# Optimization experiments

Hardware: AMD Instinct MI355X
Metric: run time of the kernel (lower is better)

The kernel has to match this reference:

```python
import jax, jax.numpy as jnp
import numpy as np

NEG_SLOPE = 0.01
EPS = 1e-8


def _conv2d(x, w, b, pad):
    y = jax.lax.conv_general_dilated(
        x, w, window_strides=(1, 1), padding=[(pad, pad), (pad, pad)],
        dimension_numbers=("NCHW", "OIHW", "NCHW"))
    return y + b[None, :, None, None]


def _leaky(x):
    return jnp.where(x >= 0, x, NEG_SLOPE * x)


def _maxpool2(x):
    return jax.lax.reduce_window(x, -jnp.inf, jax.lax.max,
                                 (1, 1, 2, 2), (1, 1, 2, 2), "VALID")


def _upsample2(x):  # nearest, scale_factor=2 (matches F.interpolate default)
    return jnp.repeat(jnp.repeat(x, 2, axis=2), 2, axis=3)


def _forward(x1, x2, pts1, enc, dec):
    B, L = pts1.shape[:2]
    H, W = x1.shape[-2:]
    h1, h2 = x1, x2
    pts = pts1.astype(jnp.int32)
    attns, feats = [], []
    for (w, b) in enc:
        Hi, Wi = h1.shape[-2:]
        h1 = _leaky(_conv2d(h1, w, b, 2))
        h2 = _leaky(_conv2d(h2, w, b, 2))
        feats.append(h2)
        h1 = _maxpool2(h1)
        h2 = _maxpool2(h2)
        C_, Hi_, Wi_ = h1.shape[-3:]
        # pts[...,0] = pts[...,0]*Hi_//Hi ; same for W (integer floor)
        pts = jnp.stack([(pts[..., 0] * Hi_) // Hi, (pts[..., 1] * Wi_) // Wi], axis=-1)
        idx = pts[..., 0] * Wi_ + pts[..., 1]  # (B, L)
        h1f = h1.reshape(B, C_, Hi_ * Wi_)
        h2f = h2.reshape(B, C_, Hi_ * Wi_)
        query = jnp.take_along_axis(h1f, jnp.broadcast_to(idx[:, None, :], (B, C_, L)), axis=2)  # (B, C, L)
        # cosine similarity between every pixel of h2 and every query point
        dots = jnp.einsum("bcp,bcl->bpl", h2f, query)
        n2 = jnp.maximum(jnp.linalg.norm(h2f, axis=1), EPS)    # (B, P)
        nq = jnp.maximum(jnp.linalg.norm(query, axis=1), EPS)  # (B, L)
        attn = dots / (n2[:, :, None] * nq[:, None, :])        # (B, P, L)
        attn = attn.reshape(B, Hi_, Wi_, L).transpose(0, 3, 1, 2).reshape(B * L, 1, Hi_, Wi_)
        attns.append(attn)
    h2 = jnp.tile(h2, (L, 1, 1, 1))  # torch .repeat(L,1,1,1)
    n_dec = len(dec)
    for i, (w, b) in enumerate(dec):
        j = len(enc) - i - 1
        h2 = jnp.concatenate([h2, attns[j]], axis=1)
        h2 = _upsample2(h2)
        feat = jnp.tile(feats[j], (L, 1, 1, 1))
        h2 = jnp.concatenate([h2, feat], axis=1)
        h2 = _conv2d(h2, w, b, 1)
        if i < n_dec - 1:
            h2 = _leaky(h2)
    return h2.reshape(B, L, H, W)


def setup_inputs() -> dict:
    key = jax.random.key(0)
    ks = jax.random.split(key, 24)
    B, L, H, W = 2, 32, 256, 256
    inp = {
        "x1": jax.random.uniform(ks[0], (B, 3, H, W), dtype=jnp.float32),
        "x2": jax.random.uniform(ks[1], (B, 3, H, W), dtype=jnp.float32),
        "pts1": jax.random.randint(ks[2], (B, L, 2), 0, H, dtype=jnp.int32),
    }
    enc_shapes = [(4, 3), (8, 4), (16, 8), (16, 16)]
    dec_shapes = [(16, 33), (8, 33), (4, 17), (1, 9)]
    k = 3
    for i, (co, ci) in enumerate(enc_shapes):
        inp[f"enc_w{i}"] = jax.random.normal(ks[k], (co, ci, 5, 5), dtype=jnp.float32) * 0.05
        inp[f"enc_b{i}"] = jnp.zeros((co,), dtype=jnp.float32)
        k += 1
    for i, (co, ci) in enumerate(dec_shapes):
        inp[f"dec_w{i}"] = jax.random.normal(ks[k], (co, ci, 3, 3), dtype=jnp.float32) * 0.05
        inp[f"dec_b{i}"] = jnp.zeros((co,), dtype=jnp.float32)
        k += 1
    return inp


def reference(x1, x2, pts1,
              enc_w0, enc_b0, enc_w1, enc_b1, enc_w2, enc_b2, enc_w3, enc_b3,
              dec_w0, dec_b0, dec_w1, dec_b1, dec_w2, dec_b2, dec_w3, dec_b3):
    enc = [(enc_w0, enc_b0), (enc_w1, enc_b1), (enc_w2, enc_b2), (enc_w3, enc_b3)]
    dec = [(dec_w0, dec_b0), (dec_w1, dec_b1), (dec_w2, dec_b2), (dec_w3, dec_b3)]
    return _forward(x1, x2, pts1, enc, dec)
```

## Files before the change

kernel.cpp:

```cpp
#include <hip/hip_runtime.h>
#include <cstdint>

__device__ __forceinline__ float leaky(float v) { return v >= 0.f ? v : 0.01f * v; }

__global__ void __launch_bounds__(256) enc0_k(
    const float* __restrict__ x1, const float* __restrict__ x2,
    const float* __restrict__ w, const float* __restrict__ bias,
    float* __restrict__ c2, float* __restrict__ pout)
{
    constexpr int R = 256;
    __shared__ float ss[3 * 36 * 36];
    __shared__ float ws[4 * 3 * 25 + 4];
    int t = threadIdx.x;
    int n = blockIdx.y;
    int tileY = blockIdx.x >> 3, tileX = blockIdx.x & 7;
    int Y0 = 32 * tileY, X0 = 32 * tileX;
    const float* src = (n < 2) ? x1 + (size_t)n * 3 * R * R
                               : x2 + (size_t)(n - 2) * 3 * R * R;

    for (int i = t; i < 300; i += 256) ws[i] = w[i];
    if (t < 4) ws[300 + t] = bias[t];
    for (int ci = 0; ci < 3; ++ci) {
        const float* sp = src + (size_t)ci * R * R;
        for (int i = t; i < 1296; i += 256) {
            int r = i / 36, col = i - r * 36;
            int gy = Y0 - 2 + r, gx = X0 - 2 + col;
            float v = 0.f;
            if (gy >= 0 && gy < R && gx >= 0 && gx < R) v = sp[gy * R + gx];
            ss[ci * 1296 + i] = v;
        }
    }
    __syncthreads();

    int qx = t & 15, qy = t >> 4;
    float acc[4][2][2];
#pragma unroll
    for (int co = 0; co < 4; ++co) {
        float b0 = ws[300 + co];
        acc[co][0][0] = b0; acc[co][0][1] = b0; acc[co][1][0] = b0; acc[co][1][1] = b0;
    }
#pragma unroll
    for (int ci = 0; ci < 3; ++ci) {
        const float* sp = &ss[ci * 1296 + (2 * qy) * 36 + 2 * qx];
        float S[6][6];
#pragma unroll
        for (int i = 0; i < 6; ++i)
#pragma unroll
            for (int j = 0; j < 6; ++j) S[i][j] = sp[i * 36 + j];
#pragma unroll
        for (int co = 0; co < 4; ++co) {
#pragma unroll
            for (int dy = 0; dy < 5; ++dy) {
#pragma unroll
                for (int dx = 0; dx < 5; ++dx) {
                    float wv = ws[(co * 3 + ci) * 25 + dy * 5 + dx];
                    acc[co][0][0] = fmaf(wv, S[dy][dx],         acc[co][0][0]);
                    acc[co][0][1] = fmaf(wv, S[dy][dx + 1],     acc[co][0][1]);
                    acc[co][1][0] = fmaf(wv, S[dy + 1][dx],     acc[co][1][0]);
                    acc[co][1][1] = fmaf(wv, S[dy + 1][dx + 1], acc[co][1][1]);
                }
            }
        }
    }
#pragma unroll
    for (int co = 0; co < 4; ++co) {
        float v00 = leaky(acc[co][0][0]), v01 = leaky(acc[co][0][1]);
        float v10 = leaky(acc[co][1][0]), v11 = leaky(acc[co][1][1]);
        if (n >= 2) {
            float* op = c2 + ((size_t)((n - 2) * 4 + co)) * R * R + (Y0 + 2 * qy) * R + X0 + 2 * qx;
            float2 a; a.x = v00; a.y = v01; *(float2*)op = a;
            float2 b2; b2.x = v10; b2.y = v11; *(float2*)(op + R) = b2;
        }
        float pv = fmaxf(fmaxf(v00, v01), fmaxf(v10, v11));
        pout[((size_t)(n * 4 + co)) * 16384 + (16 * tileY + qy) * 128 + 16 * tileX + qx] = pv;
    }
}

template<int R, int CI, int CO, int COG>
__device__ __forceinline__ void enc_body(
    const float* __restrict__ src1, const float* __restrict__ src2,
    const float* __restrict__ w, const float* __restrict__ bias,
    float* __restrict__ c2, float* __restrict__ pout, int bx)
{
    constexpr int W = R, H = R, Wt = R / 2;
    constexpr int RPB = 256 / Wt;
    __shared__ float ws[COG * CI * 25];
    __shared__ float pl[(RPB / 2) * COG * Wt];

    int t = threadIdx.x;
    int gid = bx * 256 + t;
    int col = gid % Wt;
    int y = (gid / Wt) % H;
    int n = (gid / (Wt * H)) & 3;
    int g = gid / (Wt * H * 4);

    if (COG == 2) {
        for (int i = t; i < COG * CI * 25; i += 256) {
            int cg = i & 1, idx = i >> 1;
            ws[idx * 2 + cg] = w[(g * COG + cg) * CI * 25 + idx];
        }
    } else {
        for (int i = t; i < COG * CI * 25; i += 256) ws[i] = w[g * COG * CI * 25 + i];
    }
    __syncthreads();

    const float* sp = (n < 2) ? (src1 + (size_t)n * CI * H * W)
                              : (src2 + (size_t)(n - 2) * CI * H * W);
    int x0 = col * 2;

    float acc[COG][2];
#pragma unroll
    for (int cg = 0; cg < COG; ++cg) { float b0 = bias[g * COG + cg]; acc[cg][0] = b0; acc[cg][1] = b0; }

    bool okr[5], okc[3];
#pragma unroll
    for (int i = 0; i < 5; ++i) { int yy = y + i - 2; okr[i] = (yy >= 0) && (yy < H); }
#pragma unroll
    for (int j = 0; j < 3; ++j) { int xx = x0 + 2 * j - 2; okc[j] = (xx >= 0) && (xx < W); }

#pragma unroll 4
    for (int ci = 0; ci < CI; ++ci) {
        const float* s = sp + ci * H * W + (y - 2) * W + (x0 - 2);
        float p[5][6];
#pragma unroll
        for (int i = 0; i < 5; ++i) {
#pragma unroll
            for (int j = 0; j < 3; ++j) {
                if (okr[i] & okc[j]) {
                    float2 v = *(const float2*)(s + i * W + 2 * j);
                    p[i][2 * j] = v.x; p[i][2 * j + 1] = v.y;
                } else { p[i][2 * j] = 0.f; p[i][2 * j + 1] = 0.f; }
            }
        }
        if (COG == 2) {
#pragma unroll
            for (int dy = 0; dy < 5; ++dy) {
#pragma unroll
                for (int dx = 0; dx < 5; ++dx) {
                    float2 wv = *(const float2*)&ws[(ci * 25 + dy * 5 + dx) * 2];
                    acc[0][0] = fmaf(wv.x, p[dy][dx],     acc[0][0]);
                    acc[0][1] = fmaf(wv.x, p[dy][dx + 1], acc[0][1]);
                    acc[1][0] = fmaf(wv.y, p[dy][dx],     acc[1][0]);
                    acc[1][1] = fmaf(wv.y, p[dy][dx + 1], acc[1][1]);
                }
            }
        } else {
#pragma unroll
            for (int cg = 0; cg < COG; ++cg) {
#pragma unroll
                for (int dy = 0; dy < 5; ++dy) {
#pragma unroll
                    for (int dx = 0; dx < 5; ++dx) {
                        float wv = ws[(cg * CI + ci) * 25 + dy * 5 + dx];
                        acc[cg][0] = fmaf(wv, p[dy][dx],     acc[cg][0]);
                        acc[cg][1] = fmaf(wv, p[dy][dx + 1], acc[cg][1]);
                    }
                }
            }
        }
    }

    int r = t / Wt;
    float m[COG];
#pragma unroll
    for (int cg = 0; cg < COG; ++cg) {
        float v0 = leaky(acc[cg][0]), v1 = leaky(acc[cg][1]);
        m[cg] = fmaxf(v0, v1);
        if (n >= 2) {
            float2 stv; stv.x = v0; stv.y = v1;
            *(float2*)(c2 + ((size_t)((n - 2) * CO + g * COG + cg)) * H * W + y * W + x0) = stv;
        }
    }
    if (r & 1) {
#pragma unroll
        for (int cg = 0; cg < COG; ++cg)
            pl[((r >> 1) * COG + cg) * Wt + col] = m[cg];
    }
    __syncthreads();
    if (!(r & 1)) {
#pragma unroll
        for (int cg = 0; cg < COG; ++cg) {
            float pv = fmaxf(m[cg], pl[((r >> 1) * COG + cg) * Wt + col]);
            pout[((size_t)(n * CO + g * COG + cg)) * Wt * Wt + (y >> 1) * Wt + col] = pv;
        }
    }
}

template<int R, int CI, int CO, int COG>
__global__ void __launch_bounds__(256) enc_k(
    const float* __restrict__ src1, const float* __restrict__ src2,
    const float* __restrict__ w, const float* __restrict__ bias,
    float* __restrict__ c2, float* __restrict__ pout)
{
    enc_body<R, CI, CO, COG>(src1, src2, w, bias, c2, pout, blockIdx.x);
}

template<int C, int RP, int SHIFT>
__device__ __forceinline__ void attn_body(
    const float* __restrict__ pool, const int* __restrict__ pts,
    float* __restrict__ out, int tile, int b)
{
    constexpr int P = RP * RP;
    __shared__ float qs[32 * C];
    int t = threadIdx.x;
    if (t < 32) {
        int l = t;
        int py = pts[(b * 32 + l) * 2 + 0] >> SHIFT;
        int px = pts[(b * 32 + l) * 2 + 1] >> SHIFT;
        const float* qp = pool + (size_t)(b * C) * P + py * RP + px;
        float v[C]; float s = 0.f;
#pragma unroll
        for (int c = 0; c < C; ++c) { v[c] = qp[c * P]; s += v[c] * v[c]; }
        float invn = 1.f / fmaxf(sqrtf(s), 1e-8f);
#pragma unroll
        for (int c = 0; c < C; ++c) qs[l * C + c] = v[c] * invn;
    }
    __syncthreads();
    int p = tile * 256 + t;
    const float* hp = pool + (size_t)((2 + b) * C) * P + p;
    float v[C]; float s = 0.f;
#pragma unroll
    for (int c = 0; c < C; ++c) { v[c] = hp[c * P]; s += v[c] * v[c]; }
    float invn2 = 1.f / fmaxf(sqrtf(s), 1e-8f);
#pragma unroll 4
    for (int l = 0; l < 32; ++l) {
        float d = 0.f;
#pragma unroll
        for (int c = 0; c < C; ++c) d = fmaf(v[c], qs[l * C + c], d);
        out[(size_t)(b * 32 + l) * P + p] = d * invn2;
    }
}

template<int R, int CI, int CINW, int CO, int COG>
__device__ __forceinline__ void fb_body(
    const float* __restrict__ in, const float* __restrict__ w,
    const float* __restrict__ bias, float* __restrict__ fb,
    int par, int tile, int cog)
{
    constexpr int QD = R / 2;
    __shared__ float ws[COG * CI * 9];
    int t = threadIdx.x;
    for (int i = t; i < COG * CI * 9; i += 256) {
        int co = i / (CI * 9), rem = i - co * (CI * 9);
        ws[i] = w[(cog * COG + co) * CINW * 9 + (CINW - CI) * 9 + rem];
    }
    __syncthreads();
    int q = tile * 256 + t;
    int qx = q % QD, qy = q / QD;
    const float* ip = in + (size_t)par * CI * R * R;
    float acc[COG][2][2];
#pragma unroll
    for (int co = 0; co < COG; ++co) {
        float b0 = bias[cog * COG + co];
        acc[co][0][0] = b0; acc[co][0][1] = b0; acc[co][1][0] = b0; acc[co][1][1] = b0;
    }
    bool fr[4], fc[4];
#pragma unroll
    for (int i = 0; i < 4; ++i) {
        int yy = 2 * qy - 1 + i; fr[i] = (yy >= 0) && (yy < R);
        int xx = 2 * qx - 1 + i; fc[i] = (xx >= 0) && (xx < R);
    }
#pragma unroll 4
    for (int ci = 0; ci < CI; ++ci) {
        const float* bp = ip + (size_t)ci * R * R + (2 * qy - 1) * R + (2 * qx - 1);
        float F[4][4];
#pragma unroll
        for (int i = 0; i < 4; ++i)
#pragma unroll
            for (int j = 0; j < 4; ++j)
                F[i][j] = (fr[i] & fc[j]) ? bp[i * R + j] : 0.f;
#pragma unroll
        for (int co = 0; co < COG; ++co) {
#pragma unroll
            for (int dy = 0; dy < 3; ++dy) {
#pragma unroll
                for (int dx = 0; dx < 3; ++dx) {
                    float wv = ws[(co * CI + ci) * 9 + dy * 3 + dx];
                    acc[co][0][0] = fmaf(wv, F[dy][dx],         acc[co][0][0]);
                    acc[co][0][1] = fmaf(wv, F[dy][dx + 1],     acc[co][0][1]);
                    acc[co][1][0] = fmaf(wv, F[dy + 1][dx],     acc[co][1][0]);
                    acc[co][1][1] = fmaf(wv, F[dy + 1][dx + 1], acc[co][1][1]);
                }
            }
        }
    }
#pragma unroll
    for (int co = 0; co < COG; ++co) {
        float* op = fb + ((size_t)(par * CO + cog * COG + co)) * R * R + (2 * qy) * R + 2 * qx;
        float2 a; a.x = acc[co][0][0]; a.y = acc[co][0][1]; *(float2*)op = a;
        float2 b2; b2.x = acc[co][1][0]; b2.y = acc[co][1][1]; *(float2*)(op + R) = b2;
    }
}

__device__ __forceinline__ void fb0_body(
    const float* __restrict__ p3, const float* __restrict__ c2_3,
    const float* __restrict__ w, const float* __restrict__ bias,
    float* __restrict__ fb0, int par, int tile, int cog)
{
    __shared__ float ws0[4 * 33 * 9];
    int t = threadIdx.x;
    for (int i = t; i < 4 * 33 * 9; i += 256) ws0[i] = w[cog * 4 * 33 * 9 + i];
    __syncthreads();
    int px = tile * 256 + t;
    int x = px & 31, y = px >> 5;
    const float* prevp = p3 + (size_t)(2 + par) * 16 * 256;
    const float* featp = c2_3 + (size_t)par * 16 * 1024;
    float acc[4];
#pragma unroll
    for (int co = 0; co < 4; ++co) acc[co] = bias[cog * 4 + co];

    bool oky[3], okx[3];
    int py[3], pxh[3];
#pragma unroll
    for (int i = 0; i < 3; ++i) {
        int iy = y - 1 + i; oky[i] = (iy >= 0) && (iy < 32); py[i] = (iy >= 0 ? iy : 0) >> 1;
        int ix = x - 1 + i; okx[i] = (ix >= 0) && (ix < 32); pxh[i] = (ix >= 0 ? ix : 0) >> 1;
    }
#pragma unroll 4
    for (int ci = 0; ci < 16; ++ci) {
        const float* pp = prevp + ci * 256;
        float V[3][3];
#pragma unroll
        for (int i = 0; i < 3; ++i)
#pragma unroll
            for (int j = 0; j < 3; ++j)
                V[i][j] = (oky[i] & okx[j]) ? pp[py[i] * 16 + pxh[j]] : 0.f;
#pragma unroll
        for (int co = 0; co < 4; ++co) {
#pragma unroll
            for (int tap = 0; tap < 9; ++tap)
                acc[co] = fmaf(ws0[(co * 33 + ci) * 9 + tap], V[tap / 3][tap % 3], acc[co]);
        }
    }
#pragma unroll 4
    for (int cf = 0; cf < 16; ++cf) {
        const float* fp = featp + cf * 1024;
        float F[3][3];
#pragma unroll
        for (int i = 0; i < 3; ++i)
#pragma unroll
            for (int j = 0; j < 3; ++j) {
                int iy = y - 1 + i, ix = x - 1 + j;
                F[i][j] = (oky[i] & okx[j]) ? fp[iy * 32 + ix] : 0.f;
            }
#pragma unroll
        for (int co = 0; co < 4; ++co) {
#pragma unroll
            for (int tap = 0; tap < 9; ++tap)
                acc[co] = fmaf(ws0[(co * 33 + 17 + cf) * 9 + tap], F[tap / 3][tap % 3], acc[co]);
        }
    }
#pragma unroll
    for (int co = 0; co < 4; ++co)
        fb0[((size_t)(par * 16 + cog * 4 + co)) * 1024 + y * 32 + x] = acc[co];
}

__global__ void __launch_bounds__(256) bigprep_k(
    const float* __restrict__ p0, const float* __restrict__ p1,
    const float* __restrict__ p2, const int* __restrict__ pts,
    const float* __restrict__ ew3, const float* __restrict__ eb3,
    float* __restrict__ c2_3, float* __restrict__ p3,
    const float* __restrict__ c2_0, const float* __restrict__ c2_1,
    const float* __restrict__ c2_2,
    const float* __restrict__ dw1, const float* __restrict__ db1,
    const float* __restrict__ dw2, const float* __restrict__ db2,
    const float* __restrict__ dw3, const float* __restrict__ db3,
    float* __restrict__ at0, float* __restrict__ at1, float* __restrict__ at2,
    float* __restrict__ fb1, float* __restrict__ fb2, float* __restrict__ fb3)
{
    int bx = blockIdx.x;
    if (bx < 128) {
        enc_body<32, 16, 16, 1>(p2, p2 + (size_t)2 * 16 * 32 * 32, ew3, eb3, c2_3, p3, bx);
    } else if (bx < 256) {
        int r = bx - 128; attn_body<4, 128, 1>(p0, pts, at0, r >> 1, r & 1);
    } else if (bx < 288) {
        int r = bx - 256; attn_body<8, 64, 2>(p1, pts, at1, r >> 1, r & 1);
    } else if (bx < 296) {
        int r = bx - 288; attn_body<16, 32, 3>(p2, pts, at2, r >> 1, r & 1);
    } else if (bx < 424) {
        int sub = bx - 296; int par = sub >> 6, tile = sub & 63;
        fb_body<256, 4, 9, 1, 1>(c2_0, dw3, db3, fb3, par, tile, 0);
    } else if (bx < 456) {
        int sub = bx - 424; int par = sub >> 4, tile = sub & 15;
        fb_body<128, 8, 17, 4, 4>(c2_1, dw2, db2, fb2, par, tile, 0);
    } else {
        int sub = bx - 456; int cog = sub & 1, tile = (sub >> 1) & 3, par = sub >> 3;
        fb_body<64, 16, 33, 8, 4>(c2_2, dw1, db1, fb1, par, tile, cog);
    }
}

__global__ void __launch_bounds__(256) prep2_k(
    const float* __restrict__ p3, const float* __restrict__ c2_3,
    const int* __restrict__ pts,
    const float* __restrict__ dw0, const float* __restrict__ db0,
    float* __restrict__ at3, float* __restrict__ fb0)
{
    int bx = blockIdx.x;
    if (bx < 2) {
        attn_body<16, 16, 4>(p3, pts, at3, bx >> 1, bx & 1);
    } else {
        int sub = bx - 2; int cog = sub & 3, tile = (sub >> 2) & 3, par = sub >> 4;
        fb0_body(p3, c2_3, dw0, db0, fb0, par, tile, cog);
    }
}

__global__ void __launch_bounds__(256) dec0k_k(
    const float* __restrict__ at3, const float* __restrict__ fb0,
    const float* __restrict__ w, float* __restrict__ out)
{
    __shared__ float ws4[9 * 16];
    int t = threadIdx.x;
    if (t < 144) {
        int tap = t / 16, co = t - (t / 16) * 16;
        ws4[tap * 16 + co] = w[co * 33 * 9 + 16 * 9 + tap];
    }
    __syncthreads();
    int gid = blockIdx.x;
    int k = gid >> 2, tile = gid & 3;
    int px = tile * 256 + t;
    int x = px & 31, y = px >> 5;
    int par = k & 1;
    const float* ap = at3 + (size_t)k * 256;

    float A[3][3];
#pragma unroll
    for (int i = 0; i < 3; ++i) {
        int iy = y - 1 + i; bool oy = (iy >= 0) && (iy < 32); int py = (iy >= 0 ? iy : 0) >> 1;
#pragma unroll
        for (int j = 0; j < 3; ++j) {
            int ix = x - 1 + j; bool ox = (ix >= 0) && (ix < 32); int qx = (ix >= 0 ? ix : 0) >> 1;
            A[i][j] = (oy && ox) ? ap[py * 16 + qx] : 0.f;
        }
    }
    float acc[16];
#pragma unroll
    for (int co = 0; co < 16; ++co)
        acc[co] = fb0[((size_t)(par * 16 + co)) * 1024 + y * 32 + x];
#pragma unroll
    for (int tap = 0; tap < 9; ++tap) {
        float av = A[tap / 3][tap % 3];
#pragma unroll
        for (int c4 = 0; c4 < 4; ++c4) {
            float4 wv = *(const float4*)&ws4[tap * 16 + c4 * 4];
            acc[c4 * 4 + 0] = fmaf(wv.x, av, acc[c4 * 4 + 0]);
            acc[c4 * 4 + 1] = fmaf(wv.y, av, acc[c4 * 4 + 1]);
            acc[c4 * 4 + 2] = fmaf(wv.z, av, acc[c4 * 4 + 2]);
            acc[c4 * 4 + 3] = fmaf(wv.w, av, acc[c4 * 4 + 3]);
        }
    }
#pragma unroll
    for (int co = 0; co < 16; ++co)
        out[((size_t)(k * 16 + co)) * 1024 + y * 32 + x] = leaky(acc[co]);
}

__global__ void __launch_bounds__(256, 4) dec1k_k(
    const float* __restrict__ prev, const float* __restrict__ attn,
    const float* __restrict__ fb1, const float* __restrict__ w,
    float* __restrict__ out)
{
    constexpr int R = 64, CP = 16, CIN = 33, Rh = 32, CO = 8, COG = 4;
    __shared__ float ws[17 * 9 * COG];
    __shared__ float sh4[17 * 60 * 4];

    int t = threadIdx.x;
    int bz = blockIdx.y;
    int kg = bz >> 1, cog = bz & 1;
    int p = kg & 1;
    int kbase = (kg >> 1) * 8 + p;
    int tileY = blockIdx.x >> 2, tileX = blockIdx.x & 3;
    int Y0 = 8 * tileY, X0 = 16 * tileX;
    int hy0 = 4 * tileY - 1, hx0 = 8 * tileX - 1;

    for (int i = t; i < 17 * 9 * COG; i += 256) {
        int col = i & 3, idx = i >> 2;
        ws[idx * 4 + col] = w[(cog * COG + col) * CIN * 9 + idx];
    }
#pragma unroll 2
    for (int i = t; i < 17 * 60; i += 256) {
        int c = i / 60, rem = i - c * 60;
        int r = rem / 10, col = rem - r * 10;
        int gy = hy0 + r, gx = hx0 + col;
        bool ok = (gy >= 0) && (gy < Rh) && (gx >= 0) && (gx < Rh);
        int off = gy * Rh + gx;
        float4 v4; v4.x = 0.f; v4.y = 0.f; v4.z = 0.f; v4.w = 0.f;
        if (ok) {
            if (c < CP) {
                v4.x = prev[((size_t)((kbase + 0) * CP + c)) * Rh * Rh + off];
                v4.y = prev[((size_t)((kbase + 2) * CP + c)) * Rh * Rh + off];
                v4.z = prev[((size_t)((kbase + 4) * CP + c)) * Rh * Rh + off];
                v4.w = prev[((size_t)((kbase + 6) * CP + c)) * Rh * Rh + off];
            } else {
                v4.x = attn[(size_t)(kbase + 0) * Rh * Rh + off];
                v4.y = attn[(size_t)(kbase + 2) * Rh * Rh + off];
                v4.z = attn[(size_t)(kbase + 4) * Rh * Rh + off];
                v4.w = attn[(size_t)(kbase + 6) * Rh * Rh + off];
            }
        }
        *(float4*)&sh4[i * 4] = v4;
    }
    __syncthreads();

    int px = t & 127, copair = t >> 7;
    int qx = px & 15, qy = px >> 4;

    float acc[4][2];
#pragma unroll
    for (int c2 = 0; c2 < 2; ++c2) {
        float fv = fb1[((size_t)(p * CO + cog * COG + copair * 2 + c2)) * 4096 + (Y0 + qy) * R + X0 + qx];
#pragma unroll
        for (int j = 0; j < 4; ++j) acc[j][c2] = fv;
    }

    int rr[3] = {(qy + 1) >> 1, (qy + 2) >> 1, (qy + 3) >> 1};
    int cc[3] = {(qx + 1) >> 1, (qx + 2) >> 1, (qx + 3) >> 1};
    int pofs[3][3];
#pragma unroll
    for (int i = 0; i < 3; ++i)
#pragma unroll
        for (int j2 = 0; j2 < 3; ++j2)
            pofs[i][j2] = (rr[i] * 10 + cc[j2]) * 4;

#pragma unroll 4
    for (int ci = 0; ci < 17; ++ci) {
        const float* hp = &sh4[ci * 240];
        float4 P4[3][3];
#pragma unroll
        for (int i = 0; i < 3; ++i)
#pragma unroll
            for (int j2 = 0; j2 < 3; ++j2)
                P4[i][j2] = *(const float4*)&hp[pofs[i][j2]];
#pragma unroll
        for (int dy = 0; dy < 3; ++dy) {
#pragma unroll
            for (int dx = 0; dx < 3; ++dx) {
                float2 wv = *(const float2*)&ws[(ci * 9 + dy * 3 + dx) * 4 + copair * 2];
                acc[0][0] = fmaf(wv.x, P4[dy][dx].x, acc[0][0]);
                acc[1][0] = fmaf(wv.x, P4[dy][dx].y, acc[1][0]);
                acc[2][0] = fmaf(wv.x, P4[dy][dx].z, acc[2][0]);
                acc[3][0] = fmaf(wv.x, P4[dy][dx].w, acc[3][0]);
                acc[0][1] = fmaf(wv.y, P4[dy][dx].x, acc[0][1]);
                acc[1][1] = fmaf(wv.y, P4[dy][dx].y, acc[1][1]);
                acc[2][1] = fmaf(wv.y, P4[dy][dx].z, acc[2][1]);
                acc[3][1] = fmaf(wv.y, P4[dy][dx].w, acc[3][1]);
            }
        }
    }

#pragma unroll
    for (int j = 0; j < 4; ++j) {
        int k = kbase + 2 * j;
#pragma unroll
        for (int c2 = 0; c2 < 2; ++c2) {
            int co = cog * COG + copair * 2 + c2;
            out[((size_t)(k * CO + co)) * 4096 + (Y0 + qy) * R + X0 + qx] = leaky(acc[j][c2]);
        }
    }
}

template<int R, int CP, int CO, int CINW, int MINW, bool DOLEAKY>
__global__ void __launch_bounds__(256, MINW) dechalf_k(
    const float* __restrict__ prev, const float* __restrict__ attn,
    const float* __restrict__ fb, const float* __restrict__ w,
    float* __restrict__ out)
{
    constexpr int Rh = R / 2, TX = R / 16;
    constexpr bool PACKW = (CO == 4);
    __shared__ float sh[4][(CP + 1) * 100];
    __shared__ float ws4[PACKW ? (CP + 1) * 9 * 4 : 4];

    int t = threadIdx.x;
    int kg = blockIdx.y;
    int p = kg & 1;
    int kbase = (kg >> 1) * 8 + p;
    int tileY = blockIdx.x / TX, tileX = blockIdx.x % TX;
    int Y0 = 16 * tileY, X0 = 16 * tileX;
    int hy0 = 8 * tileY - 1, hx0 = 8 * tileX - 1;

    if (PACKW) {
        for (int i = t; i < (CP + 1) * 9 * 4; i += 256) {
            int co = i & 3, idx = i >> 2;
            ws4[i] = w[co * CINW * 9 + idx];
        }
    }
#pragma unroll 2
    for (int i = t; i < CP * 100; i += 256) {
        int c = i / 100, rem = i - c * 100;
        int r = rem / 10, col = rem - r * 10;
        int gy = hy0 + r, gx = hx0 + col;
        bool ok = (gy >= 0) && (gy < Rh) && (gx >= 0) && (gx < Rh);
        int off = gy * Rh + gx;
#pragma unroll
        for (int j = 0; j < 4; ++j) {
            float v = 0.f;
            if (ok) v = prev[((size_t)((kbase + 2 * j) * CP + c)) * Rh * Rh + off];
            sh[j][i] = v;
        }
    }
    if (t < 100) {
        int r = t / 10, col = t - r * 10;
        int gy = hy0 + r, gx = hx0 + col;
        bool ok = (gy >= 0) && (gy < Rh) && (gx >= 0) && (gx < Rh);
        int off = gy * Rh + gx;
#pragma unroll
        for (int j = 0; j < 4; ++j) {
            float v = 0.f;
            if (ok) v = attn[(size_t)(kbase + 2 * j) * Rh * Rh + off];
            sh[j][CP * 100 + t] = v;
        }
    }
    __syncthreads();

    int ksub = t >> 6, q = t & 63, qx = q & 7, qy = q >> 3;
    int k = kbase + 2 * ksub;

    float acc[CO][2][2];
#pragma unroll
    for (int co = 0; co < CO; ++co) {
        const float* fp = fb + ((size_t)(p * CO + co)) * R * R + (Y0 + 2 * qy) * R + X0 + 2 * qx;
        float2 r0 = *(const float2*)fp;
        float2 r1 = *(const float2*)(fp + R);
        acc[co][0][0] = r0.x; acc[co][0][1] = r0.y;
        acc[co][1][0] = r1.x; acc[co][1][1] = r1.y;
    }

#pragma unroll
    for (int ci = 0; ci < CP + 1; ++ci) {
        const float* hp = &sh[ksub][ci * 100 + qy * 10 + qx];
        float P[3][3];
#pragma unroll
        for (int i = 0; i < 3; ++i)
#pragma unroll
            for (int j = 0; j < 3; ++j) P[i][j] = hp[i * 10 + j];
#pragma unroll
        for (int dy = 0; dy < 3; ++dy) {
#pragma unroll
            for (int dx = 0; dx < 3; ++dx) {
                float p00 = P[(dy + 1) >> 1][(dx + 1) >> 1];
                float p01 = P[(dy + 1) >> 1][(dx + 2) >> 1];
                float p10 = P[(dy + 2) >> 1][(dx + 1) >> 1];
                float p11 = P[(dy + 2) >> 1][(dx + 2) >> 1];
                if (PACKW) {
                    float4 wv = *(const float4*)&ws4[(ci * 9 + dy * 3 + dx) * 4];
                    const float* wvp = (const float*)&wv;
#pragma unroll
                    for (int co = 0; co < CO; ++co) {
                        acc[co][0][0] = fmaf(wvp[co], p00, acc[co][0][0]);
                        acc[co][0][1] = fmaf(wvp[co], p01, acc[co][0][1]);
                        acc[co][1][0] = fmaf(wvp[co], p10, acc[co][1][0]);
                        acc[co][1][1] = fmaf(wvp[co], p11, acc[co][1][1]);
                    }
                } else {
                    float wv = w[ci * 9 + dy * 3 + dx];
                    acc[0][0][0] = fmaf(wv, p00, acc[0][0][0]);
                    acc[0][0][1] = fmaf(wv, p01, acc[0][0][1]);
                    acc[0][1][0] = fmaf(wv, p10, acc[0][1][0]);
                    acc[0][1][1] = fmaf(wv, p11, acc[0][1][1]);
                }
            }
        }
    }

#pragma unroll
    for (int co = 0; co < CO; ++co) {
        float v00 = acc[co][0][0], v01 = acc[co][0][1];
        float v10 = acc[co][1][0], v11 = acc[co][1][1];
        if (DOLEAKY) { v00 = leaky(v00); v01 = leaky(v01); v10 = leaky(v10); v11 = leaky(v11); }
        float* op = out + ((size_t)(k * CO + co)) * R * R + (Y0 + 2 * qy) * R + X0 + 2 * qx;
        float2 a; a.x = v00; a.y = v01; *(float2*)op = a;
        float2 b2; b2.x = v10; b2.y = v11; *(float2*)(op + R) = b2;
    }
}

extern "C" void kernel_launch(void* const* d_in, const int* in_sizes, int n_in,
                              void* d_out, int out_size, void* d_ws, size_t ws_size,
                              hipStream_t stream)
{
    (void)in_sizes; (void)n_in; (void)out_size; (void)ws_size;
    const float* x1 = (const float*)d_in[0];
    const float* x2 = (const float*)d_in[1];
    const int* pts = (const int*)d_in[2];
    const float* ew[4] = {(const float*)d_in[3], (const float*)d_in[5],
                          (const float*)d_in[7], (const float*)d_in[9]};
    const float* eb[4] = {(const float*)d_in[4], (const float*)d_in[6],
                          (const float*)d_in[8], (const float*)d_in[10]};
    const float* dw[4] = {(const float*)d_in[11], (const float*)d_in[13],
                          (const float*)d_in[15], (const float*)d_in[17]};
    const float* db[4] = {(const float*)d_in[12], (const float*)d_in[14],
                          (const float*)d_in[16], (const float*)d_in[18]};

    float* wsp = (float*)d_ws;
    size_t off = 0;
    auto A = [&](size_t n) { float* p = wsp + off; off += n; return p; };

    float* p0 = A((size_t)4 * 4 * 128 * 128);
    float* p1 = A((size_t)4 * 8 * 64 * 64);
    float* p2 = A((size_t)4 * 16 * 32 * 32);
    float* p3 = A((size_t)4 * 16 * 16 * 16);
    float* c2_0 = A((size_t)2 * 4 * 256 * 256);
    float* c2_1 = A((size_t)2 * 8 * 128 * 128);
    float* c2_2 = A((size_t)2 * 16 * 64 * 64);
    float* c2_3 = A((size_t)2 * 16 * 32 * 32);
    float* at0 = A((size_t)64 * 128 * 128);
    float* at1 = A((size_t)64 * 64 * 64);
    float* at2 = A((size_t)64 * 32 * 32);
    float* at3 = A((size_t)64 * 16 * 16);
    float* dec0 = A((size_t)64 * 16 * 32 * 32);
    float* dec1 = A((size_t)64 * 8 * 64 * 64);
    float* dec2 = A((size_t)64 * 4 * 128 * 128);
    float* fb0 = A((size_t)2 * 16 * 32 * 32);
    float* fb1 = A((size_t)2 * 8 * 64 * 64);
    float* fb2 = A((size_t)2 * 4 * 128 * 128);
    float* fb3 = A((size_t)2 * 256 * 256);
    float* outp = (float*)d_out;

    { dim3 g(64, 4); enc0_k<<<g, 256, 0, stream>>>(x1, x2, ew[0], eb[0], c2_0, p0); }
    enc_k<128, 4, 8, 2><<<512, 256, 0, stream>>>(p0, p0 + (size_t)2 * 4 * 128 * 128,
                                                 ew[1], eb[1], c2_1, p1);
    enc_k<64, 8, 16, 2><<<256, 256, 0, stream>>>(p1, p1 + (size_t)2 * 8 * 64 * 64,
                                                 ew[2], eb[2], c2_2, p2);

    bigprep_k<<<472, 256, 0, stream>>>(p0, p1, p2, pts, ew[3], eb[3], c2_3, p3,
                                       c2_0, c2_1, c2_2,
                                       dw[1], db[1], dw[2], db[2], dw[3], db[3],
                                       at0, at1, at2, fb1, fb2, fb3);

    prep2_k<<<34, 256, 0, stream>>>(p3, c2_3, pts, dw[0], db[0], at3, fb0);

    dec0k_k<<<256, 256, 0, stream>>>(at3, fb0, dw[0], dec0);
    { dim3 g(32, 32); dec1k_k<<<g, 256, 0, stream>>>(dec0, at2, fb1, dw[1], dec1); }
    { dim3 g(64, 16); dechalf_k<128, 8, 4, 17, 4, true><<<g, 256, 0, stream>>>(dec1, at1, fb2, dw[2], dec2); }
    { dim3 g(256, 16); dechalf_k<256, 4, 1, 9, 5, false><<<g, 256, 0, stream>>>(dec2, at0, fb3, dw[3], outp); }
}
```

Baseline: 130.9 us.

## Stage encoder conv tiles in shared memory with 4-channel output groups

Encoder layers 1 and 2 now use a new kernel. Each block loads a 16x16 output tile plus a 2-pixel halo for all input channels into shared memory. Each thread computes one pixel for 4 output channels using float4 weight loads, and the 2x2 max-pool is done through shared memory. This replaces direct global loads, where each thread read overlapping 5x6 windows and covered 2 output channels. The change aims to cut redundant global traffic and raise arithmetic reuse, at the cost of more blocks, extra syncs and lower per-thread work. The old enc_k wrapper is removed and the COG==2 special case in enc_body is simplified.

```diff
diff --git a/kernel.cpp b/kernel.cpp
--- a/kernel.cpp
+++ b/kernel.cpp
@@ -76,6 +76,86 @@
     }
 }
 
+template<int R, int CI, int CO, int COG, int NCOG>
+__global__ void __launch_bounds__(256) enc_staged_k(
+    const float* __restrict__ pin, const float* __restrict__ w,
+    const float* __restrict__ bias, float* __restrict__ c2, float* __restrict__ pout)
+{
+    constexpr int TILES = R / 16, Wt = R / 2;
+    __shared__ float ss[CI * 400];
+    __shared__ float ws4[CI * 25 * COG];
+    __shared__ float pe[COG * 256];
+
+    int t = threadIdx.x;
+    int by = blockIdx.y;
+    int n = by / NCOG, cog = by % NCOG;
+    int tileY = blockIdx.x / TILES, tileX = blockIdx.x % TILES;
+    int Y0 = 16 * tileY, X0 = 16 * tileX;
+
+    for (int i = t; i < CI * 25 * COG; i += 256) {
+        int cg = i % COG, idx = i / COG;
+        ws4[idx * COG + cg] = w[(cog * COG + cg) * CI * 25 + idx];
+    }
+    const float* base = pin + (size_t)n * CI * R * R;
+#pragma unroll 2
+    for (int i = t; i < CI * 400; i += 256) {
+        int c = i / 400, rem = i - c * 400;
+        int r = rem / 20, col = rem - r * 20;
+        int gy = Y0 - 2 + r, gx = X0 - 2 + col;
+        float v = 0.f;
+        if (gy >= 0 && gy < R && gx >= 0 && gx < R)
+            v = base[(size_t)c * R * R + gy * R + gx];
+        ss[i] = v;
+    }
+    __syncthreads();
+
+    int qx = t & 15, qy = t >> 4;
+    float acc[COG];
+#pragma unroll
+    for (int cg = 0; cg < COG; ++cg) acc[cg] = bias[cog * COG + cg];
+
+#pragma unroll 4
+    for (int ci = 0; ci < CI; ++ci) {
+        const float* sp = &ss[ci * 400 + qy * 20 + qx];
+        float S[5][5];
+#pragma unroll
+        for (int i = 0; i < 5; ++i)
+#pragma unroll
+            for (int j = 0; j < 5; ++j) S[i][j] = sp[i * 20 + j];
+#pragma unroll
+        for (int dy = 0; dy < 5; ++dy) {
+#pragma unroll
+            for (int dx = 0; dx < 5; ++dx) {
+                float4 wv = *(const float4*)&ws4[(ci * 25 + dy * 5 + dx) * COG];
+                float sv = S[dy][dx];
+                acc[0] = fmaf(wv.x, sv, acc[0]);
+                acc[1] = fmaf(wv.y, sv, acc[1]);
+                acc[2] = fmaf(wv.z, sv, acc[2]);
+                acc[3] = fmaf(wv.w, sv, acc[3]);
+            }
+        }
+    }
+
+#pragma unroll
+    for (int cg = 0; cg < COG; ++cg) {
+        float v = leaky(acc[cg]);
+        if (n >= 2)
+            c2[((size_t)((n - 2) * CO + cog * COG + cg)) * R * R + (Y0 + qy) * R + X0 + qx] = v;
+        pe[cg * 256 + t] = v;
+    }
+    __syncthreads();
+    if (t < 64) {
+        int py = t >> 3, px = t & 7;
+        int b0 = (2 * py) * 16 + 2 * px;
+#pragma unroll
+        for (int cg = 0; cg < COG; ++cg) {
+            const float* pp = &pe[cg * 256];
+            float pv = fmaxf(fmaxf(pp[b0], pp[b0 + 1]), fmaxf(pp[b0 + 16], pp[b0 + 17]));
+            pout[((size_t)(n * CO + cog * COG + cg)) * Wt * Wt + (8 * tileY + py) * Wt + 8 * tileX + px] = pv;
+        }
+    }
+}
+
 template<int R, int CI, int CO, int COG>
 __device__ __forceinline__ void enc_body(
     const float* __restrict__ src1, const float* __restrict__ src2,
@@ -94,14 +174,7 @@
     int n = (gid / (Wt * H)) & 3;
     int g = gid / (Wt * H * 4);
 
-    if (COG == 2) {
-        for (int i = t; i < COG * CI * 25; i += 256) {
-            int cg = i & 1, idx = i >> 1;
-            ws[idx * 2 + cg] = w[(g * COG + cg) * CI * 25 + idx];
-        }
-    } else {
-        for (int i = t; i < COG * CI * 25; i += 256) ws[i] = w[g * COG * CI * 25 + i];
-    }
+    for (int i = t; i < COG * CI * 25; i += 256) ws[i] = w[g * COG * CI * 25 + i];
     __syncthreads();
 
     const float* sp = (n < 2) ? (src1 + (size_t)n * CI * H * W)
@@ -132,29 +205,15 @@
                 } else { p[i][2 * j] = 0.f; p[i][2 * j + 1] = 0.f; }
             }
         }
-        if (COG == 2) {
+#pragma unroll
+        for (int cg = 0; cg < COG; ++cg) {
 #pragma unroll
             for (int dy = 0; dy < 5; ++dy) {
 #pragma unroll
                 for (int dx = 0; dx < 5; ++dx) {
-                    float2 wv = *(const float2*)&ws[(ci * 25 + dy * 5 + dx) * 2];
-                    acc[0][0] = fmaf(wv.x, p[dy][dx],     acc[0][0]);
-                    acc[0][1] = fmaf(wv.x, p[dy][dx + 1], acc[0][1]);
-                    acc[1][0] = fmaf(wv.y, p[dy][dx],     acc[1][0]);
-                    acc[1][1] = fmaf(wv.y, p[dy][dx + 1], acc[1][1]);
-                }
-            }
-        } else {
-#pragma unroll
-            for (int cg = 0; cg < COG; ++cg) {
-#pragma unroll
-                for (int dy = 0; dy < 5; ++dy) {
-#pragma unroll
-                    for (int dx = 0; dx < 5; ++dx) {
-                        float wv = ws[(cg * CI + ci) * 25 + dy * 5 + dx];
-                        acc[cg][0] = fmaf(wv, p[dy][dx],     acc[cg][0]);
-                        acc[cg][1] = fmaf(wv, p[dy][dx + 1], acc[cg][1]);
-                    }
+                    float wv = ws[(cg * CI + ci) * 25 + dy * 5 + dx];
+                    acc[cg][0] = fmaf(wv, p[dy][dx],     acc[cg][0]);
+                    acc[cg][1] = fmaf(wv, p[dy][dx + 1], acc[cg][1]);
                 }
             }
         }
@@ -184,15 +243,6 @@
             pout[((size_t)(n * CO + g * COG + cg)) * Wt * Wt + (y >> 1) * Wt + col] = pv;
         }
     }
-}
-
-template<int R, int CI, int CO, int COG>
-__global__ void __launch_bounds__(256) enc_k(
-    const float* __restrict__ src1, const float* __restrict__ src2,
-    const float* __restrict__ w, const float* __restrict__ bias,
-    float* __restrict__ c2, float* __restrict__ pout)
-{
-    enc_body<R, CI, CO, COG>(src1, src2, w, bias, c2, pout, blockIdx.x);
 }
 
 template<int C, int RP, int SHIFT>
@@ -714,10 +764,8 @@
     float* outp = (float*)d_out;
 
     { dim3 g(64, 4); enc0_k<<<g, 256, 0, stream>>>(x1, x2, ew[0], eb[0], c2_0, p0); }
-    enc_k<128, 4, 8, 2><<<512, 256, 0, stream>>>(p0, p0 + (size_t)2 * 4 * 128 * 128,
-                                                 ew[1], eb[1], c2_1, p1);
-    enc_k<64, 8, 16, 2><<<256, 256, 0, stream>>>(p1, p1 + (size_t)2 * 8 * 64 * 64,
-                                                 ew[2], eb[2], c2_2, p2);
+    { dim3 g(64, 8); enc_staged_k<128, 4, 8, 4, 2><<<g, 256, 0, stream>>>(p0, ew[1], eb[1], c2_1, p1); }
+    { dim3 g(16, 16); enc_staged_k<64, 8, 16, 4, 4><<<g, 256, 0, stream>>>(p1, ew[2], eb[2], c2_2, p2); }
 
     bigprep_k<<<472, 256, 0, stream>>>(p0, p1, p2, pts, ew[3], eb[3], c2_3, p3,
                                        c2_0, c2_1, c2_2,
```

Result: slower. 139.8 us (+6.9%).

## Fold nearest-upsample into parity-collapsed 2x2 weights for decoder convs

Applied to the files above, without the earlier changes.

Because a 3x3 conv applied after nearest 2x upsampling only ever reads a 2x2 window of the low-resolution input, each output parity class can use precomputed summed weights over 4 taps instead of 9. The decoder kernels build these parity-combined weights in shared memory and do 4 FMAs per channel instead of 9. The half-resolution kernel is also restructured so each thread handles one pixel across 4 batch copies, using float4-packed shared tiles. The cost is a small per-block weight precompute and different floating-point summation order.

```diff
diff --git a/kernel.cpp b/kernel.cpp
--- a/kernel.cpp
+++ b/kernel.cpp
@@ -453,14 +453,26 @@
         out[((size_t)(k * 16 + co)) * 1024 + y * 32 + x] = leaky(acc[co]);
 }
 
+__device__ __forceinline__ float parity_wsum(const float* wp, int py, int pxr, int ti, int tj)
+{
+    int dy0 = (py == 0) ? (ti == 0 ? 0 : 1) : (ti == 0 ? 0 : 2);
+    int dy1 = (py == 0) ? (ti == 0 ? 0 : 2) : (ti == 0 ? 1 : 2);
+    int dx0 = (pxr == 0) ? (tj == 0 ? 0 : 1) : (tj == 0 ? 0 : 2);
+    int dx1 = (pxr == 0) ? (tj == 0 ? 0 : 2) : (tj == 0 ? 1 : 2);
+    float s = 0.f;
+    for (int dy = dy0; dy <= dy1; ++dy)
+        for (int dx = dx0; dx <= dx1; ++dx) s += wp[dy * 3 + dx];
+    return s;
+}
+
 __global__ void __launch_bounds__(256, 4) dec1k_k(
     const float* __restrict__ prev, const float* __restrict__ attn,
     const float* __restrict__ fb1, const float* __restrict__ w,
     float* __restrict__ out)
 {
-    constexpr int R = 64, CP = 16, CIN = 33, Rh = 32, CO = 8, COG = 4;
-    __shared__ float ws[17 * 9 * COG];
-    __shared__ float sh4[17 * 60 * 4];
+    constexpr int R = 64, CP = 16, CIN = 33, Rh = 32, CO = 8, COG = 4, NCI = 17;
+    __shared__ float wc[NCI * 16 * COG];
+    __shared__ float sh4[NCI * 60 * 4];
 
     int t = threadIdx.x;
     int bz = blockIdx.y;
@@ -471,12 +483,13 @@
     int Y0 = 8 * tileY, X0 = 16 * tileX;
     int hy0 = 4 * tileY - 1, hx0 = 8 * tileX - 1;
 
-    for (int i = t; i < 17 * 9 * COG; i += 256) {
-        int col = i & 3, idx = i >> 2;
-        ws[idx * 4 + col] = w[(cog * COG + col) * CIN * 9 + idx];
+    for (int i = t; i < NCI * 16 * COG; i += 256) {
+        int co = i & 3, tap = (i >> 2) & 3, par = (i >> 4) & 3, ci = i >> 6;
+        const float* wp = &w[(cog * COG + co) * CIN * 9 + ci * 9];
+        wc[i] = parity_wsum(wp, par >> 1, par & 1, tap >> 1, tap & 1);
     }
 #pragma unroll 2
-    for (int i = t; i < 17 * 60; i += 256) {
+    for (int i = t; i < NCI * 60; i += 256) {
         int c = i / 60, rem = i - c * 60;
         int r = rem / 10, col = rem - r * 10;
         int gy = hy0 + r, gx = hx0 + col;
@@ -502,6 +515,9 @@
 
     int px = t & 127, copair = t >> 7;
     int qx = px & 15, qy = px >> 4;
+    int par = (qy & 1) * 2 + (qx & 1);
+    int rb = (qy + 1) >> 1, cb = (qx + 1) >> 1;
+    int o00 = (rb * 10 + cb) * 4;
 
     float acc[4][2];
 #pragma unroll
@@ -511,39 +527,34 @@
         for (int j = 0; j < 4; ++j) acc[j][c2] = fv;
     }
 
-    int rr[3] = {(qy + 1) >> 1, (qy + 2) >> 1, (qy + 3) >> 1};
-    int cc[3] = {(qx + 1) >> 1, (qx + 2) >> 1, (qx + 3) >> 1};
-    int pofs[3][3];
-#pragma unroll
-    for (int i = 0; i < 3; ++i)
-#pragma unroll
-        for (int j2 = 0; j2 < 3; ++j2)
-            pofs[i][j2] = (rr[i] * 10 + cc[j2]) * 4;
-
 #pragma unroll 4
-    for (int ci = 0; ci < 17; ++ci) {
+    for (int ci = 0; ci < NCI; ++ci) {
         const float* hp = &sh4[ci * 240];
-        float4 P4[3][3];
-#pragma unroll
-        for (int i = 0; i < 3; ++i)
-#pragma unroll
-            for (int j2 = 0; j2 < 3; ++j2)
-                P4[i][j2] = *(const float4*)&hp[pofs[i][j2]];
-#pragma unroll
-        for (int dy = 0; dy < 3; ++dy) {
-#pragma unroll
-            for (int dx = 0; dx < 3; ++dx) {
-                float2 wv = *(const float2*)&ws[(ci * 9 + dy * 3 + dx) * 4 + copair * 2];
-                acc[0][0] = fmaf(wv.x, P4[dy][dx].x, acc[0][0]);
-                acc[1][0] = fmaf(wv.x, P4[dy][dx].y, acc[1][0]);
-                acc[2][0] = fmaf(wv.x, P4[dy][dx].z, acc[2][0]);
-                acc[3][0] = fmaf(wv.x, P4[dy][dx].w, acc[3][0]);
-                acc[0][1] = fmaf(wv.y, P4[dy][dx].x, acc[0][1]);
-                acc[1][1] = fmaf(wv.y, P4[dy][dx].y, acc[1][1]);
-                acc[2][1] = fmaf(wv.y, P4[dy][dx].z, acc[2][1]);
-                acc[3][1] = fmaf(wv.y, P4[dy][dx].w, acc[3][1]);
-            }
-        }
+        float4 P00 = *(const float4*)&hp[o00];
+        float4 P01 = *(const float4*)&hp[o00 + 4];
+        float4 P10 = *(const float4*)&hp[o00 + 40];
+        float4 P11 = *(const float4*)&hp[o00 + 44];
+        const float* wb = &wc[(ci * 4 + par) * 16 + copair * 2];
+        float2 w0 = *(const float2*)&wb[0];
+        float2 w1 = *(const float2*)&wb[4];
+        float2 w2 = *(const float2*)&wb[8];
+        float2 w3 = *(const float2*)&wb[12];
+        acc[0][0] = fmaf(w0.x, P00.x, acc[0][0]); acc[0][0] = fmaf(w1.x, P01.x, acc[0][0]);
+        acc[0][0] = fmaf(w2.x, P10.x, acc[0][0]); acc[0][0] = fmaf(w3.x, P11.x, acc[0][0]);
+        acc[1][0] = fmaf(w0.x, P00.y, acc[1][0]); acc[1][0] = fmaf(w1.x, P01.y, acc[1][0]);
+        acc[1][0] = fmaf(w2.x, P10.y, acc[1][0]); acc[1][0] = fmaf(w3.x, P11.y, acc[1][0]);
+        acc[2][0] = fmaf(w0.x, P00.z, acc[2][0]); acc[2][0] = fmaf(w1.x, P01.z, acc[2][0]);
+        acc[2][0] = fmaf(w2.x, P10.z, acc[2][0]); acc[2][0] = fmaf(w3.x, P11.z, acc[2][0]);
+        acc[3][0] = fmaf(w0.x, P00.w, acc[3][0]); acc[3][0] = fmaf(w1.x, P01.w, acc[3][0]);
+        acc[3][0] = fmaf(w2.x, P10.w, acc[3][0]); acc[3][0] = fmaf(w3.x, P11.w, acc[3][0]);
+        acc[0][1] = fmaf(w0.y, P00.x, acc[0][1]); acc[0][1] = fmaf(w1.y, P01.x, acc[0][1]);
+        acc[0][1] = fmaf(w2.y, P10.x, acc[0][1]); acc[0][1] = fmaf(w3.y, P11.x, acc[0][1]);
+        acc[1][1] = fmaf(w0.y, P00.y, acc[1][1]); acc[1][1] = fmaf(w1.y, P01.y, acc[1][1]);
+        acc[1][1] = fmaf(w2.y, P10.y, acc[1][1]); acc[1][1] = fmaf(w3.y, P11.y, acc[1][1]);
+        acc[2][1] = fmaf(w0.y, P00.z, acc[2][1]); acc[2][1] = fmaf(w1.y, P01.z, acc[2][1]);
+        acc[2][1] = fmaf(w2.y, P10.z, acc[2][1]); acc[2][1] = fmaf(w3.y, P11.z, acc[2][1]);
+        acc[3][1] = fmaf(w0.y, P00.w, acc[3][1]); acc[3][1] = fmaf(w1.y, P01.w, acc[3][1]);
+        acc[3][1] = fmaf(w2.y, P10.w, acc[3][1]); acc[3][1] = fmaf(w3.y, P11.w, acc[3][1]);
     }
 
 #pragma unroll
@@ -558,15 +569,15 @@
 }
 
 template<int R, int CP, int CO, int CINW, int MINW, bool DOLEAKY>
-__global__ void __launch_bounds__(256, MINW) dechalf_k(
+__global__ void __launch_bounds__(256, MINW) dechalf2_k(
     const float* __restrict__ prev, const float* __restrict__ attn,
     const float* __restrict__ fb, const float* __restrict__ w,
     float* __restrict__ out)
 {
-    constexpr int Rh = R / 2, TX = R / 16;
-    constexpr bool PACKW = (CO == 4);
-    __shared__ float sh[4][(CP + 1) * 100];
-    __shared__ float ws4[PACKW ? (CP + 1) * 9 * 4 : 4];
+    constexpr int Rh = R / 2, TX = R / 16, NCI = CP + 1;
+    constexpr int NW = (CO == 4) ? NCI * 16 * 4 : NCI * 16;
+    __shared__ float sh4[NCI * 100 * 4];
+    __shared__ float wc[NW];
 
     int t = threadIdx.x;
     int kg = blockIdx.y;
@@ -576,98 +587,96 @@
     int Y0 = 16 * tileY, X0 = 16 * tileX;
     int hy0 = 8 * tileY - 1, hx0 = 8 * tileX - 1;
 
-    if (PACKW) {
-        for (int i = t; i < (CP + 1) * 9 * 4; i += 256) {
-            int co = i & 3, idx = i >> 2;
-            ws4[i] = w[co * CINW * 9 + idx];
-        }
+    for (int i = t; i < NW; i += 256) {
+        int co, tap, par, ci;
+        if (CO == 4) { co = i & 3; tap = (i >> 2) & 3; par = (i >> 4) & 3; ci = i >> 6; }
+        else         { co = 0;     tap = i & 3;        par = (i >> 2) & 3; ci = i >> 4; }
+        const float* wp = &w[co * CINW * 9 + ci * 9];
+        wc[i] = parity_wsum(wp, par >> 1, par & 1, tap >> 1, tap & 1);
     }
 #pragma unroll 2
-    for (int i = t; i < CP * 100; i += 256) {
+    for (int i = t; i < NCI * 100; i += 256) {
         int c = i / 100, rem = i - c * 100;
         int r = rem / 10, col = rem - r * 10;
         int gy = hy0 + r, gx = hx0 + col;
         bool ok = (gy >= 0) && (gy < Rh) && (gx >= 0) && (gx < Rh);
         int off = gy * Rh + gx;
-#pragma unroll
-        for (int j = 0; j < 4; ++j) {
-            float v = 0.f;
-            if (ok) v = prev[((size_t)((kbase + 2 * j) * CP + c)) * Rh * Rh + off];
-            sh[j][i] = v;
-        }
-    }
-    if (t < 100) {
-        int r = t / 10, col = t - r * 10;
-        int gy = hy0 + r, gx = hx0 + col;
-        bool ok = (gy >= 0) && (gy < Rh) && (gx >= 0) && (gx < Rh);
-        int off = gy * Rh + gx;
-#pragma unroll
-        for (int j = 0; j < 4; ++j) {
-            float v = 0.f;
-            if (ok) v = attn[(size_t)(kbase + 2 * j) * Rh * Rh + off];
-            sh[j][CP * 100 + t] = v;
-        }
-    }
-    __syncthreads();
-
-    int ksub = t >> 6, q = t & 63, qx = q & 7, qy = q >> 3;
-    int k = kbase + 2 * ksub;
-
-    float acc[CO][2][2];
+        float4 v4; v4.x = 0.f; v4.y = 0.f; v4.z = 0.f; v4.w = 0.f;
+        if (ok) {
+            if (c < CP) {
+                v4.x = prev[((size_t)((kbase + 0) * CP + c)) * Rh * Rh + off];
+                v4.y = prev[((size_t)((kbase + 2) * CP + c)) * Rh * Rh + off];
+                v4.z = prev[((size_t)((kbase + 4) * CP + c)) * Rh * Rh + off];
+                v4.w = prev[((size_t)((kbase + 6) * CP + c)) * Rh * Rh + off];
+            } else {
+                v4.x = attn[(size_t)(kbase + 0) * Rh * Rh + off];
+                v4.y = attn[(size_t)(kbase + 2) * Rh * Rh + off];
+                v4.z = attn[(size_t)(kbase + 4) * Rh * Rh + off];
+                v4.w = attn[(size_t)(kbase + 6) * Rh * Rh + off];
+            }
+        }
+        *(float4*)&sh4[i * 4] = v4;
+    }
+    __syncthreads();
+
+    int qx = t & 15, qy = t >> 4;
+    int par = (qy & 1) * 2 + (qx & 1);
+    int rb = (qy + 1) >> 1, cb = (qx + 1) >> 1;
+    int o00 = (rb * 10 + cb) * 4;
+
+    float acc[4][CO];
 #pragma unroll
     for (int co = 0; co < CO; ++co) {
-        const float* fp = fb + ((size_t)(p * CO + co)) * R * R + (Y0 + 2 * qy) * R + X0 + 2 * qx;
-        float2 r0 = *(const float2*)fp;
-        float2 r1 = *(const float2*)(fp + R);
-        acc[co][0][0] = r0.x; acc[co][0][1] = r0.y;
-        acc[co][1][0] = r1.x; acc[co][1][1] = r1.y;
-    }
-
-#pragma unroll
-    for (int ci = 0; ci < CP + 1; ++ci) {
-        const float* hp = &sh[ksub][ci * 100 + qy * 10 + qx];
-        float P[3][3];
-#pragma unroll
-        for (int i = 0; i < 3; ++i)
-#pragma unroll
-            for (int j = 0; j < 3; ++j) P[i][j] = hp[i * 10 + j];
-#pragma unroll
-        for (int dy = 0; dy < 3; ++dy) {
-#pragma unroll
-            for (int dx = 0; dx < 3; ++dx) {
-                float p00 = P[(dy + 1) >> 1][(dx + 1) >> 1];
-                float p01 = P[(dy + 1) >> 1][(dx + 2) >> 1];
-                float p10 = P[(dy + 2) >> 1][(dx + 1) >> 1];
-                float p11 = P[(dy + 2) >> 1][(dx + 2) >> 1];
-                if (PACKW) {
-                    float4 wv = *(const float4*)&ws4[(ci * 9 + dy * 3 + dx) * 4];
-                    const float* wvp = (const float*)&wv;
-#pragma unroll
-                    for (int co = 0; co < CO; ++co) {
-                        acc[co][0][0] = fmaf(wvp[co], p00, acc[co][0][0]);
-                        acc[co][0][1] = fmaf(wvp[co], p01, acc[co][0][1]);
-                        acc[co][1][0] = fmaf(wvp[co], p10, acc[co][1][0]);
-                        acc[co][1][1] = fmaf(wvp[co], p11, acc[co][1][1]);
-                    }
-                } else {
-                    float wv = w[ci * 9 + dy * 3 + dx];
-                    acc[0][0][0] = fmaf(wv, p00, acc[0][0][0]);
-                    acc[0][0][1] = fmaf(wv, p01, acc[0][0][1]);
-                    acc[0][1][0] = fmaf(wv, p10, acc[0][1][0]);
-                    acc[0][1][1] = fmaf(wv, p11, acc[0][1][1]);
+        float fv = fb[((size_t)(p * CO + co)) * R * R + (Y0 + qy) * R + X0 + qx];
+#pragma unroll
+        for (int j = 0; j < 4; ++j) acc[j][co] = fv;
+    }
+
+#pragma unroll
+    for (int ci = 0; ci < NCI; ++ci) {
+        const float* hp = &sh4[ci * 400];
+        float4 P00 = *(const float4*)&hp[o00];
+        float4 P01 = *(const float4*)&hp[o00 + 4];
+        float4 P10 = *(const float4*)&hp[o00 + 40];
+        float4 P11 = *(const float4*)&hp[o00 + 44];
+        const float* Pp[4] = {(const float*)&P00, (const float*)&P01,
+                              (const float*)&P10, (const float*)&P11};
+        if (CO == 4) {
+            const float* wb = &wc[(ci * 4 + par) * 16];
+#pragma unroll
+            for (int tap = 0; tap < 4; ++tap) {
+                float4 wv = *(const float4*)&wb[tap * 4];
+                const float* wvp = (const float*)&wv;
+                const float* pv = Pp[tap];
+#pragma unroll
+                for (int co = 0; co < CO; ++co) {
+#pragma unroll
+                    for (int j = 0; j < 4; ++j)
+                        acc[j][co] = fmaf(wvp[co], pv[j], acc[j][co]);
                 }
             }
-        }
-    }
-
-#pragma unroll
-    for (int co = 0; co < CO; ++co) {
-        float v00 = acc[co][0][0], v01 = acc[co][0][1];
-        float v10 = acc[co][1][0], v11 = acc[co][1][1];
-        if (DOLEAKY) { v00 = leaky(v00); v01 = leaky(v01); v10 = leaky(v10); v11 = leaky(v11); }
-        float* op = out + ((size_t)(k * CO + co)) * R * R + (Y0 + 2 * qy) * R + X0 + 2 * qx;
-        float2 a; a.x = v00; a.y = v01; *(float2*)op = a;
-        float2 b2; b2.x = v10; b2.y = v11; *(float2*)(op + R) = b2;
+        } else {
+            float4 wv = *(const float4*)&wc[(ci * 4 + par) * 4];
+            const float* wvp = (const float*)&wv;
+#pragma unroll
+            for (int tap = 0; tap < 4; ++tap) {
+                const float* pv = Pp[tap];
+#pragma unroll
+                for (int j = 0; j < 4; ++j)
+                    acc[j][0] = fmaf(wvp[tap], pv[j], acc[j][0]);
+            }
+        }
+    }
+
+#pragma unroll
+    for (int j = 0; j < 4; ++j) {
+        int k = kbase + 2 * j;
+#pragma unroll
+        for (int co = 0; co < CO; ++co) {
+            float v = acc[j][co];
+            if (DOLEAKY) v = leaky(v);
+            out[((size_t)(k * CO + co)) * R * R + (Y0 + qy) * R + X0 + qx] = v;
+        }
     }
 }
 
@@ -728,6 +737,6 @@
 
     dec0k_k<<<256, 256, 0, stream>>>(at3, fb0, dw[0], dec0);
     { dim3 g(32, 32); dec1k_k<<<g, 256, 0, stream>>>(dec0, at2, fb1, dw[1], dec1); }
-    { dim3 g(64, 16); dechalf_k<128, 8, 4, 17, 4, true><<<g, 256, 0, stream>>>(dec1, at1, fb2, dw[2], dec2); }
-    { dim3 g(256, 16); dechalf_k<256, 4, 1, 9, 5, false><<<g, 256, 0, stream>>>(dec2, at0, fb3, dw[3], outp); }
-}
+    { dim3 g(64, 16); dechalf2_k<128, 8, 4, 17, 4, true><<<g, 256, 0, stream>>>(dec1, at1, fb2, dw[2], dec2); }
+    { dim3 g(256, 16); dechalf2_k<256, 4, 1, 9, 5, false><<<g, 256, 0, stream>>>(dec2, at0, fb3, dw[3], outp); }
+}
```

After: 125.8 us. -3.9%, faster.
